# Kernel optimization log

Measured on AMD Instinct MI355X. Metric: run time of the kernel, lower is better.

The kernel has to match this reference:

```python
import jax, jax.numpy as jnp
import numpy as np

B, N0, N1, FD, L, H = 4, 256, 256, 128, 3, 1
NG = N0 + N1            # nodes per graph
N = B * NG              # total nodes
EPS_BN = 1e-5
EPS_SM = 1e-16


def _build_edges():
    def perm_edges(n, off):
        idx = np.arange(n)
        a = np.repeat(idx, n); b = np.tile(idx, n)
        m = a != b
        return np.stack([a[m], b[m]]) + off
    e_intra = np.concatenate([perm_edges(N0, 0), perm_edges(N1, N0)], axis=1)
    a = np.arange(N0); b = np.arange(N0, N0 + N1)
    cross1 = np.stack([np.repeat(a, N1), np.tile(b, N0)])
    cross2 = np.stack([np.repeat(b, N0), np.tile(a, N1)])
    eg = np.concatenate([e_intra, cross1, cross2], axis=1)
    tg = np.concatenate([np.zeros(e_intra.shape[1], np.int32),
                         np.ones(cross1.shape[1] + cross2.shape[1], np.int32)])
    ei = np.concatenate([eg + g * NG for g in range(B)], axis=1).astype(np.int32)
    et = np.tile(tg, B).astype(np.int32)
    return jnp.asarray(ei), jnp.asarray(et)


def setup_inputs() -> dict:
    key = jax.random.key(0)
    ks = jax.random.split(key, 8)
    edge_index, edge_type = _build_edges()
    return {
        'desc0': jax.random.normal(ks[0], (B, FD, N0), jnp.float32),
        'desc1': jax.random.normal(ks[1], (B, FD, N1), jnp.float32),
        'W': jax.random.normal(ks[2], (L, 2, FD, H * FD), jnp.float32) * (1.0 / np.sqrt(FD)),
        'q': jax.random.normal(ks[3], (L, H * FD, H), jnp.float32) * 0.1,
        'k': jax.random.normal(ks[4], (L, H * FD, H), jnp.float32) * 0.1,
        'conv_b': jnp.zeros((L, FD), jnp.float32),
        'lin_W': jax.random.normal(ks[5], (L, FD, 2 * FD), jnp.float32) * (1.0 / np.sqrt(2 * FD)),
        'lin_b': jnp.zeros((L, FD), jnp.float32),
        'gamma': jnp.ones((L, FD), jnp.float32),
        'beta': jnp.zeros((L, FD), jnp.float32),
        'edge_index': edge_index,
        'edge_type': edge_type,
    }


def _forward(desc0, desc1, W, q, k, conv_b, lin_W, lin_b, gamma, beta, edge_index, edge_type):
    # x: [B, NG, FD] -> flattened batch graph [N, FD]
    x = jnp.concatenate([desc0, desc1], axis=2)        # [B, FD, NG]
    x = jnp.transpose(x, (0, 2, 1)).reshape(N, FD)
    src, dst = edge_index[0], edge_index[1]
    nlayers = W.shape[0]
    heads = q.shape[2]
    for l in range(nlayers):
        # relation-specific node projections (equiv to per-edge bmm with weight[edge_type])
        proj = jnp.einsum('nf,rfo->nro', x, W[l])       # [N, 2, H*FD]
        out_i = proj[dst, edge_type]                    # [E, H*FD]
        out_j = proj[src, edge_type]                    # [E, H*FD]
        alpha = jax.nn.leaky_relu(out_i @ q[l] + out_j @ k[l], 0.2)  # [E, H]
        # softmax over incoming edges of each destination node (across-relation)
        amax = jax.ops.segment_max(alpha, dst, num_segments=N)
        ex = jnp.exp(alpha - amax[dst])
        denom = jax.ops.segment_sum(ex, dst, num_segments=N)
        att = ex / (denom[dst] + EPS_SM)                # [E, H]
        msg = (att[:, :, None] * out_j.reshape(-1, heads, FD)).reshape(-1, heads * FD)
        agg = jax.ops.segment_sum(msg, dst, num_segments=N).reshape(N, heads, FD)
        m1 = jax.nn.relu(agg.mean(axis=1) + conv_b[l])  # concat=False -> mean over heads
        m2 = jnp.concatenate([x, m1], axis=1) @ lin_W[l].T + lin_b[l]
        mu = m2.mean(axis=0)
        var = ((m2 - mu) ** 2).mean(axis=0)             # biased var (BatchNorm training)
        m3 = (m2 - mu) / jnp.sqrt(var + EPS_BN) * gamma[l] + beta[l]
        x = x + m3
    x = x.reshape(B, NG, FD).transpose(0, 2, 1)         # [B, FD, NG]
    return x


def reference(desc0, desc1, W, q, k, conv_b, lin_W, lin_b, gamma, beta, edge_index, edge_type):
    x = _forward(desc0, desc1, W, q, k, conv_b, lin_W, lin_b, gamma, beta, edge_index, edge_type)
    return x[:, :, :N0], x[:, :, N0:]
```

## Files before the change

kernel.cpp:

```cpp
#include <hip/hip_runtime.h>

#define FD  128
#define NN  2048

#define OFF_X     0
#define OFF_PROJ  262144
#define OFF_QS    786432
#define OFF_KS    790528
#define OFF_M2    794624
#define OFF_SUMS  1056768
#define OFF_LWT   1057536

__device__ __forceinline__ void proj_qsks(
    const float* __restrict__ W, const float* __restrict__ qv,
    const float* __restrict__ kv, float* __restrict__ ws,
    int l, int n0, int t, const float (*xs)[FD],
    float (*redp)[256], float* red)
{
    int kh = t >> 8, tp = t & 255;
    int rsel = tp >> 7, o = tp & 127;
    const float* Wl = W + ((size_t)(l*2 + rsel)*FD)*FD + o;
    float acc[4] = {0.f, 0.f, 0.f, 0.f};
    int kbase = kh * 64;
    for (int k4 = kbase; k4 < kbase + 64; k4 += 4) {
        float w0 = Wl[(k4+0)*FD], w1 = Wl[(k4+1)*FD];
        float w2 = Wl[(k4+2)*FD], w3 = Wl[(k4+3)*FD];
#pragma unroll
        for (int r = 0; r < 4; r++) {
            float4 xq = *(const float4*)&xs[r][k4];
            acc[r] += xq.x*w0 + xq.y*w1 + xq.z*w2 + xq.w*w3;
        }
    }
    if (kh == 1) {
#pragma unroll
        for (int r = 0; r < 4; r++) redp[r][tp] = acc[r];
    }
    __syncthreads();
    if (t < 256) {
#pragma unroll
        for (int r = 0; r < 4; r++) acc[r] += redp[r][tp];
#pragma unroll
        for (int r = 0; r < 4; r++)
            ws[OFF_PROJ + (size_t)(n0 + r)*256 + tp] = acc[r];

        float qq = qv[l*FD + o], kq = kv[l*FD + o];
        int lane = t & 63, w = t >> 6;
#pragma unroll
        for (int r = 0; r < 4; r++) {
            float vq = acc[r]*qq, vk = acc[r]*kq;
            for (int off = 32; off; off >>= 1) {
                vq += __shfl_xor(vq, off, 64);
                vk += __shfl_xor(vk, off, 64);
            }
            if (lane == 0) { red[w*8 + r*2] = vq; red[w*8 + r*2 + 1] = vk; }
        }
    }
    __syncthreads();
    if (t < 16) {
        int r = t & 3, rs = (t >> 2) & 1, wh = t >> 3;
        float v = red[(rs*2)*8 + r*2 + wh] + red[(rs*2 + 1)*8 + r*2 + wh];
        if (wh == 0) ws[OFF_QS + rs*NN + n0 + r] = v;
        else         ws[OFF_KS + rs*NN + n0 + r] = v;
    }
}

__global__ __launch_bounds__(512, 4) void k_pre(
    const float* __restrict__ d0, const float* __restrict__ d1,
    const float* __restrict__ W,  const float* __restrict__ qv,
    const float* __restrict__ kv, const float* __restrict__ linW,
    float* __restrict__ ws)
{
    int bid = blockIdx.x, t = threadIdx.x;
    if (bid >= 512) {
        if (bid < 536) {
            int vb = bid - 512;
#pragma unroll
            for (int i = 0; i < 8; i++) {
                int e = vb*4096 + i*512 + t;
                int l = e >> 15, rem = e & 32767;
                int o = rem >> 8, c = rem & 255;
                ws[OFF_LWT + l*32768 + c*FD + o] = linW[e];
            }
        } else {
            for (int i = t; i < 768; i += 512) ws[OFF_SUMS + i] = 0.f;
        }
        return;
    }
    __shared__ __attribute__((aligned(16))) float xs[4][FD];
    __shared__ float redp[4][256];
    __shared__ float red[32];
    int n0 = bid * 4;
    {
        int row = t >> 7, f = t & 127;
        int n = n0 + row, gg = n >> 9, ii = n & 511;
        float v = (ii < 256) ? d0[gg*32768 + f*256 + ii]
                             : d1[gg*32768 + f*256 + (ii - 256)];
        xs[row][f] = v;
        ws[OFF_X + (size_t)n*FD + f] = v;
    }
    __syncthreads();
    proj_qsks(W, qv, kv, ws, 0, n0, t, xs, redp, red);
}

__global__ __launch_bounds__(512, 4) void k_bp(
    const float* __restrict__ W,     const float* __restrict__ qv,
    const float* __restrict__ kv,    const float* __restrict__ gamma,
    const float* __restrict__ beta,  float* __restrict__ ws, int l)
{
    __shared__ float scale[FD], shift[FD];
    __shared__ __attribute__((aligned(16))) float xs[4][FD];
    __shared__ float redp[4][256];
    __shared__ float red[32];
    int bid = blockIdx.x, t = threadIdx.x;
    int lp = l - 1;
    if (t < FD) {
        float mu  = ws[OFF_SUMS + lp*256 + t] * (1.f/2048.f);
        float var = ws[OFF_SUMS + lp*256 + 128 + t] * (1.f/2048.f) - mu*mu;
        float rs  = rsqrtf(var + 1e-5f);
        float gm  = gamma[lp*FD + t], bt = beta[lp*FD + t];
        scale[t] = gm * rs;
        shift[t] = bt - mu * gm * rs;
    }
    __syncthreads();
    int n0 = bid * 4;
    {
        int row = t >> 7, f = t & 127;
        size_t e = (size_t)(n0 + row)*FD + f;
        float xv = ws[OFF_X + e] + ws[OFF_M2 + e]*scale[f] + shift[f];
        xs[row][f] = xv;
        ws[OFF_X + e] = xv;
    }
    __syncthreads();
    proj_qsks(W, qv, kv, ws, l, n0, t, xs, redp, red);
}

__global__ __launch_bounds__(512, 4) void k_attn(
    const float* __restrict__ convb, const float* __restrict__ linb,
    float* __restrict__ ws, int l)
{
    __shared__ __attribute__((aligned(16))) float att[4*512];
    __shared__ __attribute__((aligned(16))) float redB[16*4*128];
    __shared__ __attribute__((aligned(16))) float cat[4*256];
    __shared__ float r1[FD], r2[FD];

    int bid = blockIdx.x, t = threadIdx.x;
    int dstbase = bid * 4;
    int g = dstbase >> 9, dloc0 = dstbase & 511;
    int Gd = (dloc0 >= 256) ? 1 : 0;

    if (t < 256) {
        int d = t >> 6, p = t & 63;
        int dloc = dloc0 + d;
        float q0 = ws[OFF_QS + dstbase + d];
        float q1 = ws[OFF_QS + NN + dstbase + d];
        float sc[8];
#pragma unroll
        for (int j = 0; j < 8; j++) {
            int s = p + j*64;
            int ts = (s < 256) ? Gd : 1 - Gd;
            float a = (ts ? q1 : q0) + ws[OFF_KS + ts*NN + g*512 + s];
            a = a > 0.f ? a : 0.2f*a;
            sc[j] = (s == dloc) ? -1e30f : a;
        }
        float lm = sc[0];
#pragma unroll
        for (int j = 1; j < 8; j++) lm = fmaxf(lm, sc[j]);
        for (int off = 32; off; off >>= 1) lm = fmaxf(lm, __shfl_xor(lm, off, 64));
        float ex[8], lsum = 0.f;
#pragma unroll
        for (int j = 0; j < 8; j++) { ex[j] = __expf(sc[j] - lm); lsum += ex[j]; }
        for (int off = 32; off; off >>= 1) lsum += __shfl_xor(lsum, off, 64);
        float inv = 1.f / (lsum + 1e-16f);
#pragma unroll
        for (int j = 0; j < 8; j++) att[d*512 + p + j*64] = ex[j]*inv;
    } else if (t < 384) {
        r1[t - 256] = 0.f;
    } else {
        r2[t - 384] = 0.f;
    }
    __syncthreads();

    int f4 = t & 31, sq = t >> 5;
    {
        int ts = (sq < 8) ? Gd : 1 - Gd;
        const float* P = ws + OFF_PROJ + (size_t)(g*512)*256 + ts*128 + f4*4;
        float acc[4][4];
#pragma unroll
        for (int d2 = 0; d2 < 4; d2++)
#pragma unroll
            for (int j = 0; j < 4; j++) acc[d2][j] = 0.f;
        int s0 = sq * 32;
#pragma unroll 4
        for (int i = 0; i < 32; i++) {
            int s = s0 + i;
            float4 p4 = *(const float4*)&P[(size_t)s*256];
            float b0 = att[0*512 + s], b1 = att[1*512 + s];
            float b2 = att[2*512 + s], b3 = att[3*512 + s];
            acc[0][0] += b0*p4.x; acc[0][1] += b0*p4.y; acc[0][2] += b0*p4.z; acc[0][3] += b0*p4.w;
            acc[1][0] += b1*p4.x; acc[1][1] += b1*p4.y; acc[1][2] += b1*p4.z; acc[1][3] += b1*p4.w;
            acc[2][0] += b2*p4.x; acc[2][1] += b2*p4.y; acc[2][2] += b2*p4.z; acc[2][3] += b2*p4.w;
            acc[3][0] += b3*p4.x; acc[3][1] += b3*p4.y; acc[3][2] += b3*p4.z; acc[3][3] += b3*p4.w;
        }
#pragma unroll
        for (int d2 = 0; d2 < 4; d2++)
            *(float4*)&redB[(sq*4 + d2)*128 + f4*4] =
                make_float4(acc[d2][0], acc[d2][1], acc[d2][2], acc[d2][3]);
    }
    __syncthreads();

    {
        int d2 = t >> 7, f = t & 127;
        float agg = 0.f;
#pragma unroll
        for (int sqi = 0; sqi < 16; sqi++) agg += redB[(sqi*4 + d2)*128 + f];
        float m1v = fmaxf(agg + convb[l*FD + f], 0.f);
        cat[d2*256 + FD + f] = m1v;
        cat[d2*256 + f] = ws[OFF_X + (size_t)(dstbase + d2)*FD + f];
    }
    __syncthreads();

    {
        const float* lwt = ws + OFF_LWT + l*32768 + f4*4;
        float mac[4][4];
#pragma unroll
        for (int d2 = 0; d2 < 4; d2++)
#pragma unroll
            for (int j = 0; j < 4; j++) mac[d2][j] = 0.f;
        int c0 = sq * 16;
#pragma unroll 4
        for (int i = 0; i < 16; i++) {
            int c = c0 + i;
            float4 w4 = *(const float4*)&lwt[c*128];
            float c0v = cat[0*256 + c], c1v = cat[1*256 + c];
            float c2v = cat[2*256 + c], c3v = cat[3*256 + c];
            mac[0][0] += c0v*w4.x; mac[0][1] += c0v*w4.y; mac[0][2] += c0v*w4.z; mac[0][3] += c0v*w4.w;
            mac[1][0] += c1v*w4.x; mac[1][1] += c1v*w4.y; mac[1][2] += c1v*w4.z; mac[1][3] += c1v*w4.w;
            mac[2][0] += c2v*w4.x; mac[2][1] += c2v*w4.y; mac[2][2] += c2v*w4.z; mac[2][3] += c2v*w4.w;
            mac[3][0] += c3v*w4.x; mac[3][1] += c3v*w4.y; mac[3][2] += c3v*w4.z; mac[3][3] += c3v*w4.w;
        }
#pragma unroll
        for (int d2 = 0; d2 < 4; d2++)
            *(float4*)&redB[(sq*4 + d2)*128 + f4*4] =
                make_float4(mac[d2][0], mac[d2][1], mac[d2][2], mac[d2][3]);
    }
    __syncthreads();

    {
        int d2 = t >> 7, o = t & 127;
        float m2v = linb[l*FD + o];
#pragma unroll
        for (int sqi = 0; sqi < 16; sqi++) m2v += redB[(sqi*4 + d2)*128 + o];
        ws[OFF_M2 + (size_t)(dstbase + d2)*FD + o] = m2v;
        atomicAdd(&r1[o], m2v);
        atomicAdd(&r2[o], m2v*m2v);
    }
    __syncthreads();
    if (t < 128) {
        atomicAdd(&ws[OFF_SUMS + l*256 + t],       r1[t]);
        atomicAdd(&ws[OFF_SUMS + l*256 + 128 + t], r2[t]);
    }
}

__global__ __launch_bounds__(256) void k_bnout(
    const float* __restrict__ gamma, const float* __restrict__ beta,
    float* __restrict__ ws, float* __restrict__ out)
{
    __shared__ float scale[FD], shift[FD];
    int bid = blockIdx.x, t = threadIdx.x;
    if (t < FD) {
        float mu  = ws[OFF_SUMS + 2*256 + t] * (1.f/2048.f);
        float var = ws[OFF_SUMS + 2*256 + 128 + t] * (1.f/2048.f) - mu*mu;
        float rs  = rsqrtf(var + 1e-5f);
        float gm  = gamma[2*FD + t], bt = beta[2*FD + t];
        scale[t] = gm * rs;
        shift[t] = bt - mu * gm * rs;
    }
    __syncthreads();
#pragma unroll
    for (int i = 0; i < 2; i++) {
        int idx = bid*512 + i*256 + t;
        int f = idx & 127, n = idx >> 7;
        float v = ws[OFF_X + idx] + ws[OFF_M2 + idx]*scale[f] + shift[f];
        int gg = n >> 9, ii = n & 511;
        int off = (ii < 256) ? (gg*32768 + f*256 + ii)
                             : (131072 + gg*32768 + f*256 + (ii - 256));
        out[off] = v;
    }
}

extern "C" void kernel_launch(void* const* d_in, const int* in_sizes, int n_in,
                              void* d_out, int out_size, void* d_ws, size_t ws_size,
                              hipStream_t stream) {
    (void)in_sizes; (void)n_in; (void)out_size; (void)ws_size;
    const float* desc0 = (const float*)d_in[0];
    const float* desc1 = (const float*)d_in[1];
    const float* W     = (const float*)d_in[2];
    const float* q     = (const float*)d_in[3];
    const float* kk    = (const float*)d_in[4];
    const float* convb = (const float*)d_in[5];
    const float* linW  = (const float*)d_in[6];
    const float* linb  = (const float*)d_in[7];
    const float* gamma = (const float*)d_in[8];
    const float* beta  = (const float*)d_in[9];
    float* ws  = (float*)d_ws;
    float* out = (float*)d_out;

    hipLaunchKernelGGL(k_pre,  dim3(537), dim3(512), 0, stream, desc0, desc1, W, q, kk, linW, ws);
    hipLaunchKernelGGL(k_attn, dim3(512), dim3(512), 0, stream, convb, linb, ws, 0);
    hipLaunchKernelGGL(k_bp,   dim3(512), dim3(512), 0, stream, W, q, kk, gamma, beta, ws, 1);
    hipLaunchKernelGGL(k_attn, dim3(512), dim3(512), 0, stream, convb, linb, ws, 1);
    hipLaunchKernelGGL(k_bp,   dim3(512), dim3(512), 0, stream, W, q, kk, gamma, beta, ws, 2);
    hipLaunchKernelGGL(k_attn, dim3(512), dim3(512), 0, stream, convb, linb, ws, 2);
    hipLaunchKernelGGL(k_bnout, dim3(512), dim3(256), 0, stream, gamma, beta, ws, out);
}
```

Measured before the change: 186.6 us.

## Fuse attention, BatchNorm and next-layer projection via cooperative grid barrier

Merges the per-layer attention kernel with the following BatchNorm-apply and q/k projection into one cooperative kernel. A global atomic counter barrier waits for all blocks' BatchNorm sums, which removes separate launches and the M2 round trip through global memory. It also transposes the attention and concat buffers in shared memory so the inner loops can use float4 reads, and halves the partial-sum buffer with a two-stage reduction. The spin barrier requires all 512 blocks to be co-resident; if the cooperative launch fails, the code falls back to a split path of kernels.

```diff
diff --git a/kernel.cpp b/kernel.cpp
--- a/kernel.cpp
+++ b/kernel.cpp
@@ -7,11 +7,12 @@
 #define OFF_PROJ  262144
 #define OFF_QS    786432
 #define OFF_KS    790528
-#define OFF_M2    794624
-#define OFF_SUMS  1056768
-#define OFF_LWT   1057536
-
-__device__ __forceinline__ void proj_qsks(
+#define OFF_SUMS  794624
+#define OFF_LWT   795392
+#define OFF_M2    893696
+#define OFF_CNT   1155840
+
+__device__ __forceinline__ void proj_qsks512(
     const float* __restrict__ W, const float* __restrict__ qv,
     const float* __restrict__ kv, float* __restrict__ ws,
     int l, int n0, int t, const float (*xs)[FD],
@@ -83,6 +84,7 @@
             }
         } else {
             for (int i = t; i < 768; i += 512) ws[OFF_SUMS + i] = 0.f;
+            if (t < 3) ((unsigned*)(ws + OFF_CNT))[t] = 0u;
         }
         return;
     }
@@ -99,51 +101,14 @@
         ws[OFF_X + (size_t)n*FD + f] = v;
     }
     __syncthreads();
-    proj_qsks(W, qv, kv, ws, 0, n0, t, xs, redp, red);
-}
-
-__global__ __launch_bounds__(512, 4) void k_bp(
-    const float* __restrict__ W,     const float* __restrict__ qv,
-    const float* __restrict__ kv,    const float* __restrict__ gamma,
-    const float* __restrict__ beta,  float* __restrict__ ws, int l)
-{
-    __shared__ float scale[FD], shift[FD];
-    __shared__ __attribute__((aligned(16))) float xs[4][FD];
-    __shared__ float redp[4][256];
-    __shared__ float red[32];
-    int bid = blockIdx.x, t = threadIdx.x;
-    int lp = l - 1;
-    if (t < FD) {
-        float mu  = ws[OFF_SUMS + lp*256 + t] * (1.f/2048.f);
-        float var = ws[OFF_SUMS + lp*256 + 128 + t] * (1.f/2048.f) - mu*mu;
-        float rs  = rsqrtf(var + 1e-5f);
-        float gm  = gamma[lp*FD + t], bt = beta[lp*FD + t];
-        scale[t] = gm * rs;
-        shift[t] = bt - mu * gm * rs;
-    }
-    __syncthreads();
-    int n0 = bid * 4;
-    {
-        int row = t >> 7, f = t & 127;
-        size_t e = (size_t)(n0 + row)*FD + f;
-        float xv = ws[OFF_X + e] + ws[OFF_M2 + e]*scale[f] + shift[f];
-        xs[row][f] = xv;
-        ws[OFF_X + e] = xv;
-    }
-    __syncthreads();
-    proj_qsks(W, qv, kv, ws, l, n0, t, xs, redp, red);
-}
-
-__global__ __launch_bounds__(512, 4) void k_attn(
+    proj_qsks512(W, qv, kv, ws, 0, n0, t, xs, redp, red);
+}
+
+__device__ __forceinline__ float attn_core512(
     const float* __restrict__ convb, const float* __restrict__ linb,
-    float* __restrict__ ws, int l)
-{
-    __shared__ __attribute__((aligned(16))) float att[4*512];
-    __shared__ __attribute__((aligned(16))) float redB[16*4*128];
-    __shared__ __attribute__((aligned(16))) float cat[4*256];
-    __shared__ float r1[FD], r2[FD];
-
-    int bid = blockIdx.x, t = threadIdx.x;
+    float* __restrict__ ws, int l, int bid, int t,
+    float* attT, float* redB, float* catT, float* r1, float* r2)
+{
     int dstbase = bid * 4;
     int g = dstbase >> 9, dloc0 = dstbase & 511;
     int Gd = (dloc0 >= 256) ? 1 : 0;
@@ -172,7 +137,7 @@
         for (int off = 32; off; off >>= 1) lsum += __shfl_xor(lsum, off, 64);
         float inv = 1.f / (lsum + 1e-16f);
 #pragma unroll
-        for (int j = 0; j < 8; j++) att[d*512 + p + j*64] = ex[j]*inv;
+        for (int j = 0; j < 8; j++) attT[(p + j*64)*4 + d] = ex[j]*inv;
     } else if (t < 384) {
         r1[t - 256] = 0.f;
     } else {
@@ -181,30 +146,40 @@
     __syncthreads();
 
     int f4 = t & 31, sq = t >> 5;
+    float acc[4][4];
+#pragma unroll
+    for (int d2 = 0; d2 < 4; d2++)
+#pragma unroll
+        for (int j = 0; j < 4; j++) acc[d2][j] = 0.f;
     {
         int ts = (sq < 8) ? Gd : 1 - Gd;
         const float* P = ws + OFF_PROJ + (size_t)(g*512)*256 + ts*128 + f4*4;
-        float acc[4][4];
-#pragma unroll
-        for (int d2 = 0; d2 < 4; d2++)
-#pragma unroll
-            for (int j = 0; j < 4; j++) acc[d2][j] = 0.f;
         int s0 = sq * 32;
 #pragma unroll 4
         for (int i = 0; i < 32; i++) {
             int s = s0 + i;
             float4 p4 = *(const float4*)&P[(size_t)s*256];
-            float b0 = att[0*512 + s], b1 = att[1*512 + s];
-            float b2 = att[2*512 + s], b3 = att[3*512 + s];
-            acc[0][0] += b0*p4.x; acc[0][1] += b0*p4.y; acc[0][2] += b0*p4.z; acc[0][3] += b0*p4.w;
-            acc[1][0] += b1*p4.x; acc[1][1] += b1*p4.y; acc[1][2] += b1*p4.z; acc[1][3] += b1*p4.w;
-            acc[2][0] += b2*p4.x; acc[2][1] += b2*p4.y; acc[2][2] += b2*p4.z; acc[2][3] += b2*p4.w;
-            acc[3][0] += b3*p4.x; acc[3][1] += b3*p4.y; acc[3][2] += b3*p4.z; acc[3][3] += b3*p4.w;
-        }
+            float4 b4 = *(const float4*)&attT[s*4];
+            acc[0][0] += b4.x*p4.x; acc[0][1] += b4.x*p4.y; acc[0][2] += b4.x*p4.z; acc[0][3] += b4.x*p4.w;
+            acc[1][0] += b4.y*p4.x; acc[1][1] += b4.y*p4.y; acc[1][2] += b4.y*p4.z; acc[1][3] += b4.y*p4.w;
+            acc[2][0] += b4.z*p4.x; acc[2][1] += b4.z*p4.y; acc[2][2] += b4.z*p4.z; acc[2][3] += b4.z*p4.w;
+            acc[3][0] += b4.w*p4.x; acc[3][1] += b4.w*p4.y; acc[3][2] += b4.w*p4.z; acc[3][3] += b4.w*p4.w;
+        }
+    }
+    if (sq >= 8) {
 #pragma unroll
         for (int d2 = 0; d2 < 4; d2++)
+            *(float4*)&redB[((sq - 8)*4 + d2)*128 + f4*4] =
+                make_float4(acc[d2][0], acc[d2][1], acc[d2][2], acc[d2][3]);
+    }
+    __syncthreads();
+    if (sq < 8) {
+#pragma unroll
+        for (int d2 = 0; d2 < 4; d2++) {
+            float4 p4 = *(const float4*)&redB[(sq*4 + d2)*128 + f4*4];
             *(float4*)&redB[(sq*4 + d2)*128 + f4*4] =
-                make_float4(acc[d2][0], acc[d2][1], acc[d2][2], acc[d2][3]);
+                make_float4(acc[d2][0]+p4.x, acc[d2][1]+p4.y, acc[d2][2]+p4.z, acc[d2][3]+p4.w);
+        }
     }
     __syncthreads();
 
@@ -212,79 +187,166 @@
         int d2 = t >> 7, f = t & 127;
         float agg = 0.f;
 #pragma unroll
-        for (int sqi = 0; sqi < 16; sqi++) agg += redB[(sqi*4 + d2)*128 + f];
+        for (int sqi = 0; sqi < 8; sqi++) agg += redB[(sqi*4 + d2)*128 + f];
         float m1v = fmaxf(agg + convb[l*FD + f], 0.f);
-        cat[d2*256 + FD + f] = m1v;
-        cat[d2*256 + f] = ws[OFF_X + (size_t)(dstbase + d2)*FD + f];
-    }
-    __syncthreads();
-
+        catT[(FD + f)*4 + d2] = m1v;
+        catT[f*4 + d2]        = ws[OFF_X + (size_t)(dstbase + d2)*FD + f];
+    }
+    __syncthreads();
+
+#pragma unroll
+    for (int d2 = 0; d2 < 4; d2++)
+#pragma unroll
+        for (int j = 0; j < 4; j++) acc[d2][j] = 0.f;
     {
         const float* lwt = ws + OFF_LWT + l*32768 + f4*4;
-        float mac[4][4];
-#pragma unroll
-        for (int d2 = 0; d2 < 4; d2++)
-#pragma unroll
-            for (int j = 0; j < 4; j++) mac[d2][j] = 0.f;
         int c0 = sq * 16;
 #pragma unroll 4
         for (int i = 0; i < 16; i++) {
             int c = c0 + i;
             float4 w4 = *(const float4*)&lwt[c*128];
-            float c0v = cat[0*256 + c], c1v = cat[1*256 + c];
-            float c2v = cat[2*256 + c], c3v = cat[3*256 + c];
-            mac[0][0] += c0v*w4.x; mac[0][1] += c0v*w4.y; mac[0][2] += c0v*w4.z; mac[0][3] += c0v*w4.w;
-            mac[1][0] += c1v*w4.x; mac[1][1] += c1v*w4.y; mac[1][2] += c1v*w4.z; mac[1][3] += c1v*w4.w;
-            mac[2][0] += c2v*w4.x; mac[2][1] += c2v*w4.y; mac[2][2] += c2v*w4.z; mac[2][3] += c2v*w4.w;
-            mac[3][0] += c3v*w4.x; mac[3][1] += c3v*w4.y; mac[3][2] += c3v*w4.z; mac[3][3] += c3v*w4.w;
-        }
+            float4 c4 = *(const float4*)&catT[c*4];
+            acc[0][0] += c4.x*w4.x; acc[0][1] += c4.x*w4.y; acc[0][2] += c4.x*w4.z; acc[0][3] += c4.x*w4.w;
+            acc[1][0] += c4.y*w4.x; acc[1][1] += c4.y*w4.y; acc[1][2] += c4.y*w4.z; acc[1][3] += c4.y*w4.w;
+            acc[2][0] += c4.z*w4.x; acc[2][1] += c4.z*w4.y; acc[2][2] += c4.z*w4.z; acc[2][3] += c4.z*w4.w;
+            acc[3][0] += c4.w*w4.x; acc[3][1] += c4.w*w4.y; acc[3][2] += c4.w*w4.z; acc[3][3] += c4.w*w4.w;
+        }
+    }
+    if (sq >= 8) {
 #pragma unroll
         for (int d2 = 0; d2 < 4; d2++)
+            *(float4*)&redB[((sq - 8)*4 + d2)*128 + f4*4] =
+                make_float4(acc[d2][0], acc[d2][1], acc[d2][2], acc[d2][3]);
+    }
+    __syncthreads();
+    if (sq < 8) {
+#pragma unroll
+        for (int d2 = 0; d2 < 4; d2++) {
+            float4 p4 = *(const float4*)&redB[(sq*4 + d2)*128 + f4*4];
             *(float4*)&redB[(sq*4 + d2)*128 + f4*4] =
-                make_float4(mac[d2][0], mac[d2][1], mac[d2][2], mac[d2][3]);
-    }
-    __syncthreads();
-
-    {
-        int d2 = t >> 7, o = t & 127;
-        float m2v = linb[l*FD + o];
-#pragma unroll
-        for (int sqi = 0; sqi < 16; sqi++) m2v += redB[(sqi*4 + d2)*128 + o];
-        ws[OFF_M2 + (size_t)(dstbase + d2)*FD + o] = m2v;
-        atomicAdd(&r1[o], m2v);
-        atomicAdd(&r2[o], m2v*m2v);
-    }
+                make_float4(acc[d2][0]+p4.x, acc[d2][1]+p4.y, acc[d2][2]+p4.z, acc[d2][3]+p4.w);
+        }
+    }
+    __syncthreads();
+
+    int d2 = t >> 7, o = t & 127;
+    float m2v = linb[l*FD + o];
+#pragma unroll
+    for (int sqi = 0; sqi < 8; sqi++) m2v += redB[(sqi*4 + d2)*128 + o];
+    atomicAdd(&r1[o], m2v);
+    atomicAdd(&r2[o], m2v*m2v);
     __syncthreads();
     if (t < 128) {
         atomicAdd(&ws[OFF_SUMS + l*256 + t],       r1[t]);
         atomicAdd(&ws[OFF_SUMS + l*256 + 128 + t], r2[t]);
     }
-}
-
-__global__ __launch_bounds__(256) void k_bnout(
-    const float* __restrict__ gamma, const float* __restrict__ beta,
-    float* __restrict__ ws, float* __restrict__ out)
-{
+    return m2v;
+}
+
+__global__ __launch_bounds__(512, 4) void k_layer(
+    const float* __restrict__ W,     const float* __restrict__ qv,
+    const float* __restrict__ kv,    const float* __restrict__ convb,
+    const float* __restrict__ linb,  const float* __restrict__ gamma,
+    const float* __restrict__ beta,  float* __restrict__ ws,
+    float* __restrict__ out,         int l, int last)
+{
+    __shared__ __attribute__((aligned(16))) float attT[512*4];
+    __shared__ __attribute__((aligned(16))) float redB[8*4*128];
+    __shared__ __attribute__((aligned(16))) float catT[256*4];
+    __shared__ float r1[FD], r2[FD];
     __shared__ float scale[FD], shift[FD];
+    __shared__ float red[32];
+
     int bid = blockIdx.x, t = threadIdx.x;
-    if (t < FD) {
-        float mu  = ws[OFF_SUMS + 2*256 + t] * (1.f/2048.f);
-        float var = ws[OFF_SUMS + 2*256 + 128 + t] * (1.f/2048.f) - mu*mu;
+    float m2v = attn_core512(convb, linb, ws, l, bid, t, attT, redB, catT, r1, r2);
+    __syncthreads();
+
+    if (t == 0) {
+        __threadfence();
+        unsigned* cnt = (unsigned*)(ws + OFF_CNT) + l;
+        atomicAdd(cnt, 1u);
+        while (atomicAdd(cnt, 0u) < 512u) __builtin_amdgcn_s_sleep(8);
+    }
+    __syncthreads();
+
+    if (t < 128) {
+        float s1 = atomicAdd(&ws[OFF_SUMS + l*256 + t],       0.f);
+        float s2 = atomicAdd(&ws[OFF_SUMS + l*256 + 128 + t], 0.f);
+        float mu  = s1 * (1.f/2048.f);
+        float var = s2 * (1.f/2048.f) - mu*mu;
         float rs  = rsqrtf(var + 1e-5f);
-        float gm  = gamma[2*FD + t], bt = beta[2*FD + t];
+        float gm  = gamma[l*FD + t], bt = beta[l*FD + t];
         scale[t] = gm * rs;
         shift[t] = bt - mu * gm * rs;
     }
     __syncthreads();
-#pragma unroll
-    for (int i = 0; i < 2; i++) {
-        int idx = bid*512 + i*256 + t;
-        int f = idx & 127, n = idx >> 7;
-        float v = ws[OFF_X + idx] + ws[OFF_M2 + idx]*scale[f] + shift[f];
-        int gg = n >> 9, ii = n & 511;
-        int off = (ii < 256) ? (gg*32768 + f*256 + ii)
-                             : (131072 + gg*32768 + f*256 + (ii - 256));
-        out[off] = v;
+
+    int dstbase = bid * 4;
+    int d2 = t >> 7, o = t & 127;
+    float xnew = catT[o*4 + d2] + m2v*scale[o] + shift[o];
+    if (!last) {
+        ws[OFF_X + (size_t)(dstbase + d2)*FD + o] = xnew;
+        float (*xs)[FD] = (float (*)[FD])attT;
+        xs[d2][o] = xnew;
+        __syncthreads();
+        proj_qsks512(W, qv, kv, ws, l + 1, dstbase, t, xs,
+                     (float (*)[256])redB, red);
+    } else {
+        int n = dstbase + d2, gg = n >> 9, ii = n & 511;
+        int off = (ii < 256) ? (gg*32768 + o*256 + ii)
+                             : (131072 + gg*32768 + o*256 + (ii - 256));
+        out[off] = xnew;
+    }
+}
+
+__global__ __launch_bounds__(512, 4) void k_attn_s(
+    const float* __restrict__ convb, const float* __restrict__ linb,
+    float* __restrict__ ws, int l)
+{
+    __shared__ __attribute__((aligned(16))) float attT[512*4];
+    __shared__ __attribute__((aligned(16))) float redB[8*4*128];
+    __shared__ __attribute__((aligned(16))) float catT[256*4];
+    __shared__ float r1[FD], r2[FD];
+    int bid = blockIdx.x, t = threadIdx.x;
+    float m2v = attn_core512(convb, linb, ws, l, bid, t, attT, redB, catT, r1, r2);
+    int d2 = t >> 7, o = t & 127;
+    ws[OFF_M2 + (size_t)(bid*4 + d2)*FD + o] = m2v;
+}
+
+__global__ __launch_bounds__(512, 4) void k_bnproj(
+    const float* __restrict__ W,     const float* __restrict__ qv,
+    const float* __restrict__ kv,    const float* __restrict__ gamma,
+    const float* __restrict__ beta,  float* __restrict__ ws,
+    float* __restrict__ out,         int l, int last)
+{
+    __shared__ float scale[FD], shift[FD];
+    __shared__ __attribute__((aligned(16))) float xs[4][FD];
+    __shared__ float redp[4][256];
+    __shared__ float red[32];
+    int bid = blockIdx.x, t = threadIdx.x;
+    if (t < 128) {
+        float mu  = ws[OFF_SUMS + l*256 + t] * (1.f/2048.f);
+        float var = ws[OFF_SUMS + l*256 + 128 + t] * (1.f/2048.f) - mu*mu;
+        float rs  = rsqrtf(var + 1e-5f);
+        float gm  = gamma[l*FD + t], bt = beta[l*FD + t];
+        scale[t] = gm * rs;
+        shift[t] = bt - mu * gm * rs;
+    }
+    __syncthreads();
+    int dstbase = bid * 4;
+    int d2 = t >> 7, o = t & 127;
+    size_t e = (size_t)(dstbase + d2)*FD + o;
+    float xnew = ws[OFF_X + e] + ws[OFF_M2 + e]*scale[o] + shift[o];
+    if (!last) {
+        ws[OFF_X + e] = xnew;
+        xs[d2][o] = xnew;
+        __syncthreads();
+        proj_qsks512(W, qv, kv, ws, l + 1, dstbase, t, xs, redp, red);
+    } else {
+        int n = dstbase + d2, gg = n >> 9, ii = n & 511;
+        int off = (ii < 256) ? (gg*32768 + o*256 + ii)
+                             : (131072 + gg*32768 + o*256 + (ii - 256));
+        out[off] = xnew;
     }
 }
 
@@ -305,11 +367,31 @@
     float* ws  = (float*)d_ws;
     float* out = (float*)d_out;
 
-    hipLaunchKernelGGL(k_pre,  dim3(537), dim3(512), 0, stream, desc0, desc1, W, q, kk, linW, ws);
-    hipLaunchKernelGGL(k_attn, dim3(512), dim3(512), 0, stream, convb, linb, ws, 0);
-    hipLaunchKernelGGL(k_bp,   dim3(512), dim3(512), 0, stream, W, q, kk, gamma, beta, ws, 1);
-    hipLaunchKernelGGL(k_attn, dim3(512), dim3(512), 0, stream, convb, linb, ws, 1);
-    hipLaunchKernelGGL(k_bp,   dim3(512), dim3(512), 0, stream, W, q, kk, gamma, beta, ws, 2);
-    hipLaunchKernelGGL(k_attn, dim3(512), dim3(512), 0, stream, convb, linb, ws, 2);
-    hipLaunchKernelGGL(k_bnout, dim3(512), dim3(256), 0, stream, gamma, beta, ws, out);
-}
+    hipLaunchKernelGGL(k_pre, dim3(537), dim3(512), 0, stream,
+                       desc0, desc1, W, q, kk, linW, ws);
+
+    int l0 = 0, last0 = 0;
+    void* args0[] = { (void*)&W, (void*)&q, (void*)&kk, (void*)&convb,
+                      (void*)&linb, (void*)&gamma, (void*)&beta,
+                      (void*)&ws, (void*)&out, (void*)&l0, (void*)&last0 };
+    hipError_t err = hipLaunchCooperativeKernel((const void*)k_layer, dim3(512),
+                                                dim3(512), args0, 0, stream);
+    if (err == hipSuccess) {
+        for (int l = 1; l < 3; l++) {
+            int larg = l, lastarg = (l == 2) ? 1 : 0;
+            void* args[] = { (void*)&W, (void*)&q, (void*)&kk, (void*)&convb,
+                             (void*)&linb, (void*)&gamma, (void*)&beta,
+                             (void*)&ws, (void*)&out, (void*)&larg, (void*)&lastarg };
+            hipLaunchCooperativeKernel((const void*)k_layer, dim3(512), dim3(512),
+                                       args, 0, stream);
+        }
+    } else {
+        for (int l = 0; l < 3; l++) {
+            int lastarg = (l == 2) ? 1 : 0;
+            hipLaunchKernelGGL(k_attn_s, dim3(512), dim3(512), 0, stream,
+                               convb, linb, ws, l);
+            hipLaunchKernelGGL(k_bnproj, dim3(512), dim3(512), 0, stream,
+                               W, q, kk, gamma, beta, ws, out, l, lastarg);
+        }
+    }
+}
```

New measurement: 348.6 us. 1.87x slower.

## Process eight nodes per block with swizzled block-to-node mapping

Applied to the files above, without the earlier changes.

Each block now handles 8 destination nodes instead of 4 in the projection and attention kernels, which halves the grid to 256 blocks and doubles reuse of each loaded W, proj and linW element. The attention kernel's cross-thread reduction becomes a two-stage pairwise add in shared memory so the larger tile still fits. Block indices are swizzled so neighbouring blocks cover different graphs, and the workspace offsets are reordered. In exchange each block uses more registers and shared memory, occupancy is lowered to 2 blocks per unit, and 256 blocks may underfill a 256-CU device.

```diff
diff --git a/kernel.cpp b/kernel.cpp
--- a/kernel.cpp
+++ b/kernel.cpp
@@ -7,11 +7,17 @@
 #define OFF_PROJ  262144
 #define OFF_QS    786432
 #define OFF_KS    790528
-#define OFF_M2    794624
-#define OFF_SUMS  1056768
-#define OFF_LWT   1057536
-
-__device__ __forceinline__ void proj_qsks(
+#define OFF_SUMS  794624
+#define OFF_LWT   795392
+#define OFF_M2    893696
+
+__device__ __forceinline__ int swizzle_n0(int bid) {
+    int g    = (bid & 7) >> 1;
+    int slot = ((bid >> 3) << 1) | (bid & 1);
+    return g*512 + slot*8;
+}
+
+__device__ __forceinline__ void proj_qsks8(
     const float* __restrict__ W, const float* __restrict__ qv,
     const float* __restrict__ kv, float* __restrict__ ws,
     int l, int n0, int t, const float (*xs)[FD],
@@ -20,60 +26,62 @@
     int kh = t >> 8, tp = t & 255;
     int rsel = tp >> 7, o = tp & 127;
     const float* Wl = W + ((size_t)(l*2 + rsel)*FD)*FD + o;
-    float acc[4] = {0.f, 0.f, 0.f, 0.f};
+    float acc[8];
+#pragma unroll
+    for (int r = 0; r < 8; r++) acc[r] = 0.f;
     int kbase = kh * 64;
     for (int k4 = kbase; k4 < kbase + 64; k4 += 4) {
         float w0 = Wl[(k4+0)*FD], w1 = Wl[(k4+1)*FD];
         float w2 = Wl[(k4+2)*FD], w3 = Wl[(k4+3)*FD];
 #pragma unroll
-        for (int r = 0; r < 4; r++) {
+        for (int r = 0; r < 8; r++) {
             float4 xq = *(const float4*)&xs[r][k4];
             acc[r] += xq.x*w0 + xq.y*w1 + xq.z*w2 + xq.w*w3;
         }
     }
     if (kh == 1) {
 #pragma unroll
-        for (int r = 0; r < 4; r++) redp[r][tp] = acc[r];
+        for (int r = 0; r < 8; r++) redp[r][tp] = acc[r];
     }
     __syncthreads();
     if (t < 256) {
 #pragma unroll
-        for (int r = 0; r < 4; r++) acc[r] += redp[r][tp];
-#pragma unroll
-        for (int r = 0; r < 4; r++)
+        for (int r = 0; r < 8; r++) acc[r] += redp[r][tp];
+#pragma unroll
+        for (int r = 0; r < 8; r++)
             ws[OFF_PROJ + (size_t)(n0 + r)*256 + tp] = acc[r];
 
         float qq = qv[l*FD + o], kq = kv[l*FD + o];
         int lane = t & 63, w = t >> 6;
 #pragma unroll
-        for (int r = 0; r < 4; r++) {
+        for (int r = 0; r < 8; r++) {
             float vq = acc[r]*qq, vk = acc[r]*kq;
             for (int off = 32; off; off >>= 1) {
                 vq += __shfl_xor(vq, off, 64);
                 vk += __shfl_xor(vk, off, 64);
             }
-            if (lane == 0) { red[w*8 + r*2] = vq; red[w*8 + r*2 + 1] = vk; }
-        }
-    }
-    __syncthreads();
-    if (t < 16) {
-        int r = t & 3, rs = (t >> 2) & 1, wh = t >> 3;
-        float v = red[(rs*2)*8 + r*2 + wh] + red[(rs*2 + 1)*8 + r*2 + wh];
+            if (lane == 0) { red[w*16 + r*2] = vq; red[w*16 + r*2 + 1] = vk; }
+        }
+    }
+    __syncthreads();
+    if (t < 32) {
+        int r = t & 7, rs = (t >> 3) & 1, wh = t >> 4;
+        float v = red[(rs*2)*16 + r*2 + wh] + red[(rs*2 + 1)*16 + r*2 + wh];
         if (wh == 0) ws[OFF_QS + rs*NN + n0 + r] = v;
         else         ws[OFF_KS + rs*NN + n0 + r] = v;
     }
 }
 
-__global__ __launch_bounds__(512, 4) void k_pre(
+__global__ __launch_bounds__(512, 2) void k_pre(
     const float* __restrict__ d0, const float* __restrict__ d1,
     const float* __restrict__ W,  const float* __restrict__ qv,
     const float* __restrict__ kv, const float* __restrict__ linW,
     float* __restrict__ ws)
 {
     int bid = blockIdx.x, t = threadIdx.x;
-    if (bid >= 512) {
-        if (bid < 536) {
-            int vb = bid - 512;
+    if (bid >= 256) {
+        if (bid < 280) {
+            int vb = bid - 256;
 #pragma unroll
             for (int i = 0; i < 8; i++) {
                 int e = vb*4096 + i*512 + t;
@@ -86,12 +94,14 @@
         }
         return;
     }
-    __shared__ __attribute__((aligned(16))) float xs[4][FD];
-    __shared__ float redp[4][256];
-    __shared__ float red[32];
-    int n0 = bid * 4;
-    {
-        int row = t >> 7, f = t & 127;
+    __shared__ __attribute__((aligned(16))) float xs[8][FD];
+    __shared__ float redp[8][256];
+    __shared__ float red[64];
+    int n0 = swizzle_n0(bid);
+#pragma unroll
+    for (int i = 0; i < 2; i++) {
+        int idx = t + i*512;
+        int row = idx >> 7, f = idx & 127;
         int n = n0 + row, gg = n >> 9, ii = n & 511;
         float v = (ii < 256) ? d0[gg*32768 + f*256 + ii]
                              : d1[gg*32768 + f*256 + (ii - 256)];
@@ -99,21 +109,21 @@
         ws[OFF_X + (size_t)n*FD + f] = v;
     }
     __syncthreads();
-    proj_qsks(W, qv, kv, ws, 0, n0, t, xs, redp, red);
-}
-
-__global__ __launch_bounds__(512, 4) void k_bp(
+    proj_qsks8(W, qv, kv, ws, 0, n0, t, xs, redp, red);
+}
+
+__global__ __launch_bounds__(512, 2) void k_bp(
     const float* __restrict__ W,     const float* __restrict__ qv,
     const float* __restrict__ kv,    const float* __restrict__ gamma,
     const float* __restrict__ beta,  float* __restrict__ ws, int l)
 {
     __shared__ float scale[FD], shift[FD];
-    __shared__ __attribute__((aligned(16))) float xs[4][FD];
-    __shared__ float redp[4][256];
-    __shared__ float red[32];
+    __shared__ __attribute__((aligned(16))) float xs[8][FD];
+    __shared__ float redp[8][256];
+    __shared__ float red[64];
     int bid = blockIdx.x, t = threadIdx.x;
     int lp = l - 1;
-    if (t < FD) {
+    if (t < 128) {
         float mu  = ws[OFF_SUMS + lp*256 + t] * (1.f/2048.f);
         float var = ws[OFF_SUMS + lp*256 + 128 + t] * (1.f/2048.f) - mu*mu;
         float rs  = rsqrtf(var + 1e-5f);
@@ -122,33 +132,35 @@
         shift[t] = bt - mu * gm * rs;
     }
     __syncthreads();
-    int n0 = bid * 4;
-    {
-        int row = t >> 7, f = t & 127;
+    int n0 = swizzle_n0(bid);
+#pragma unroll
+    for (int i = 0; i < 2; i++) {
+        int idx = t + i*512;
+        int row = idx >> 7, f = idx & 127;
         size_t e = (size_t)(n0 + row)*FD + f;
         float xv = ws[OFF_X + e] + ws[OFF_M2 + e]*scale[f] + shift[f];
         xs[row][f] = xv;
         ws[OFF_X + e] = xv;
     }
     __syncthreads();
-    proj_qsks(W, qv, kv, ws, l, n0, t, xs, redp, red);
-}
-
-__global__ __launch_bounds__(512, 4) void k_attn(
+    proj_qsks8(W, qv, kv, ws, l, n0, t, xs, redp, red);
+}
+
+__global__ __launch_bounds__(512, 2) void k_attn(
     const float* __restrict__ convb, const float* __restrict__ linb,
     float* __restrict__ ws, int l)
 {
-    __shared__ __attribute__((aligned(16))) float att[4*512];
-    __shared__ __attribute__((aligned(16))) float redB[16*4*128];
-    __shared__ __attribute__((aligned(16))) float cat[4*256];
+    __shared__ __attribute__((aligned(16))) float att[8*512];
+    __shared__ __attribute__((aligned(16))) float redB[8*8*128];
+    __shared__ __attribute__((aligned(16))) float cat[8*256];
     __shared__ float r1[FD], r2[FD];
 
     int bid = blockIdx.x, t = threadIdx.x;
-    int dstbase = bid * 4;
+    int dstbase = swizzle_n0(bid);
     int g = dstbase >> 9, dloc0 = dstbase & 511;
     int Gd = (dloc0 >= 256) ? 1 : 0;
 
-    if (t < 256) {
+    {
         int d = t >> 6, p = t & 63;
         int dloc = dloc0 + d;
         float q0 = ws[OFF_QS + dstbase + d];
@@ -173,86 +185,114 @@
         float inv = 1.f / (lsum + 1e-16f);
 #pragma unroll
         for (int j = 0; j < 8; j++) att[d*512 + p + j*64] = ex[j]*inv;
-    } else if (t < 384) {
-        r1[t - 256] = 0.f;
-    } else {
-        r2[t - 384] = 0.f;
+        if (t < 128) r1[t] = 0.f;
+        else if (t < 256) r2[t - 128] = 0.f;
     }
     __syncthreads();
 
     int f4 = t & 31, sq = t >> 5;
+    float acc[8][4];
+#pragma unroll
+    for (int d2 = 0; d2 < 8; d2++)
+#pragma unroll
+        for (int j = 0; j < 4; j++) acc[d2][j] = 0.f;
     {
         int ts = (sq < 8) ? Gd : 1 - Gd;
         const float* P = ws + OFF_PROJ + (size_t)(g*512)*256 + ts*128 + f4*4;
-        float acc[4][4];
-#pragma unroll
-        for (int d2 = 0; d2 < 4; d2++)
-#pragma unroll
-            for (int j = 0; j < 4; j++) acc[d2][j] = 0.f;
         int s0 = sq * 32;
 #pragma unroll 4
         for (int i = 0; i < 32; i++) {
             int s = s0 + i;
             float4 p4 = *(const float4*)&P[(size_t)s*256];
-            float b0 = att[0*512 + s], b1 = att[1*512 + s];
-            float b2 = att[2*512 + s], b3 = att[3*512 + s];
-            acc[0][0] += b0*p4.x; acc[0][1] += b0*p4.y; acc[0][2] += b0*p4.z; acc[0][3] += b0*p4.w;
-            acc[1][0] += b1*p4.x; acc[1][1] += b1*p4.y; acc[1][2] += b1*p4.z; acc[1][3] += b1*p4.w;
-            acc[2][0] += b2*p4.x; acc[2][1] += b2*p4.y; acc[2][2] += b2*p4.z; acc[2][3] += b2*p4.w;
-            acc[3][0] += b3*p4.x; acc[3][1] += b3*p4.y; acc[3][2] += b3*p4.z; acc[3][3] += b3*p4.w;
-        }
-#pragma unroll
-        for (int d2 = 0; d2 < 4; d2++)
-            *(float4*)&redB[(sq*4 + d2)*128 + f4*4] =
+#pragma unroll
+            for (int d2 = 0; d2 < 8; d2++) {
+                float b = att[d2*512 + s];
+                acc[d2][0] += b*p4.x; acc[d2][1] += b*p4.y;
+                acc[d2][2] += b*p4.z; acc[d2][3] += b*p4.w;
+            }
+        }
+    }
+    if (sq >= 8) {
+#pragma unroll
+        for (int d2 = 0; d2 < 8; d2++)
+            *(float4*)&redB[((sq - 8)*8 + d2)*128 + f4*4] =
                 make_float4(acc[d2][0], acc[d2][1], acc[d2][2], acc[d2][3]);
     }
     __syncthreads();
-
-    {
-        int d2 = t >> 7, f = t & 127;
-        float agg = 0.f;
-#pragma unroll
-        for (int sqi = 0; sqi < 16; sqi++) agg += redB[(sqi*4 + d2)*128 + f];
-        float m1v = fmaxf(agg + convb[l*FD + f], 0.f);
-        cat[d2*256 + FD + f] = m1v;
-        cat[d2*256 + f] = ws[OFF_X + (size_t)(dstbase + d2)*FD + f];
-    }
-    __syncthreads();
-
+    if (sq < 8) {
+#pragma unroll
+        for (int d2 = 0; d2 < 8; d2++) {
+            float4 p4 = *(const float4*)&redB[(sq*8 + d2)*128 + f4*4];
+            *(float4*)&redB[(sq*8 + d2)*128 + f4*4] =
+                make_float4(acc[d2][0]+p4.x, acc[d2][1]+p4.y, acc[d2][2]+p4.z, acc[d2][3]+p4.w);
+        }
+    }
+    __syncthreads();
+
+    {
+        int dh = t >> 7, f = t & 127;
+#pragma unroll
+        for (int half = 0; half < 2; half++) {
+            int d2 = dh + half*4;
+            float agg = 0.f;
+#pragma unroll
+            for (int cc = 0; cc < 8; cc++) agg += redB[(cc*8 + d2)*128 + f];
+            float m1v = fmaxf(agg + convb[l*FD + f], 0.f);
+            cat[d2*256 + FD + f] = m1v;
+            cat[d2*256 + f] = ws[OFF_X + (size_t)(dstbase + d2)*FD + f];
+        }
+    }
+    __syncthreads();
+
+#pragma unroll
+    for (int d2 = 0; d2 < 8; d2++)
+#pragma unroll
+        for (int j = 0; j < 4; j++) acc[d2][j] = 0.f;
     {
         const float* lwt = ws + OFF_LWT + l*32768 + f4*4;
-        float mac[4][4];
-#pragma unroll
-        for (int d2 = 0; d2 < 4; d2++)
-#pragma unroll
-            for (int j = 0; j < 4; j++) mac[d2][j] = 0.f;
         int c0 = sq * 16;
 #pragma unroll 4
         for (int i = 0; i < 16; i++) {
             int c = c0 + i;
             float4 w4 = *(const float4*)&lwt[c*128];
-            float c0v = cat[0*256 + c], c1v = cat[1*256 + c];
-            float c2v = cat[2*256 + c], c3v = cat[3*256 + c];
-            mac[0][0] += c0v*w4.x; mac[0][1] += c0v*w4.y; mac[0][2] += c0v*w4.z; mac[0][3] += c0v*w4.w;
-            mac[1][0] += c1v*w4.x; mac[1][1] += c1v*w4.y; mac[1][2] += c1v*w4.z; mac[1][3] += c1v*w4.w;
-            mac[2][0] += c2v*w4.x; mac[2][1] += c2v*w4.y; mac[2][2] += c2v*w4.z; mac[2][3] += c2v*w4.w;
-            mac[3][0] += c3v*w4.x; mac[3][1] += c3v*w4.y; mac[3][2] += c3v*w4.z; mac[3][3] += c3v*w4.w;
-        }
-#pragma unroll
-        for (int d2 = 0; d2 < 4; d2++)
-            *(float4*)&redB[(sq*4 + d2)*128 + f4*4] =
-                make_float4(mac[d2][0], mac[d2][1], mac[d2][2], mac[d2][3]);
-    }
-    __syncthreads();
-
-    {
-        int d2 = t >> 7, o = t & 127;
-        float m2v = linb[l*FD + o];
-#pragma unroll
-        for (int sqi = 0; sqi < 16; sqi++) m2v += redB[(sqi*4 + d2)*128 + o];
-        ws[OFF_M2 + (size_t)(dstbase + d2)*FD + o] = m2v;
-        atomicAdd(&r1[o], m2v);
-        atomicAdd(&r2[o], m2v*m2v);
+#pragma unroll
+            for (int d2 = 0; d2 < 8; d2++) {
+                float cv = cat[d2*256 + c];
+                acc[d2][0] += cv*w4.x; acc[d2][1] += cv*w4.y;
+                acc[d2][2] += cv*w4.z; acc[d2][3] += cv*w4.w;
+            }
+        }
+    }
+    if (sq >= 8) {
+#pragma unroll
+        for (int d2 = 0; d2 < 8; d2++)
+            *(float4*)&redB[((sq - 8)*8 + d2)*128 + f4*4] =
+                make_float4(acc[d2][0], acc[d2][1], acc[d2][2], acc[d2][3]);
+    }
+    __syncthreads();
+    if (sq < 8) {
+#pragma unroll
+        for (int d2 = 0; d2 < 8; d2++) {
+            float4 p4 = *(const float4*)&redB[(sq*8 + d2)*128 + f4*4];
+            *(float4*)&redB[(sq*8 + d2)*128 + f4*4] =
+                make_float4(acc[d2][0]+p4.x, acc[d2][1]+p4.y, acc[d2][2]+p4.z, acc[d2][3]+p4.w);
+        }
+    }
+    __syncthreads();
+
+    {
+        int dh = t >> 7, o = t & 127;
+        float lb = linb[l*FD + o];
+#pragma unroll
+        for (int half = 0; half < 2; half++) {
+            int d2 = dh + half*4;
+            float m2v = lb;
+#pragma unroll
+            for (int cc = 0; cc < 8; cc++) m2v += redB[(cc*8 + d2)*128 + o];
+            ws[OFF_M2 + (size_t)(dstbase + d2)*FD + o] = m2v;
+            atomicAdd(&r1[o], m2v);
+            atomicAdd(&r2[o], m2v*m2v);
+        }
     }
     __syncthreads();
     if (t < 128) {
@@ -267,7 +307,7 @@
 {
     __shared__ float scale[FD], shift[FD];
     int bid = blockIdx.x, t = threadIdx.x;
-    if (t < FD) {
+    if (t < 128) {
         float mu  = ws[OFF_SUMS + 2*256 + t] * (1.f/2048.f);
         float var = ws[OFF_SUMS + 2*256 + 128 + t] * (1.f/2048.f) - mu*mu;
         float rs  = rsqrtf(var + 1e-5f);
@@ -305,11 +345,11 @@
     float* ws  = (float*)d_ws;
     float* out = (float*)d_out;
 
-    hipLaunchKernelGGL(k_pre,  dim3(537), dim3(512), 0, stream, desc0, desc1, W, q, kk, linW, ws);
-    hipLaunchKernelGGL(k_attn, dim3(512), dim3(512), 0, stream, convb, linb, ws, 0);
-    hipLaunchKernelGGL(k_bp,   dim3(512), dim3(512), 0, stream, W, q, kk, gamma, beta, ws, 1);
-    hipLaunchKernelGGL(k_attn, dim3(512), dim3(512), 0, stream, convb, linb, ws, 1);
-    hipLaunchKernelGGL(k_bp,   dim3(512), dim3(512), 0, stream, W, q, kk, gamma, beta, ws, 2);
-    hipLaunchKernelGGL(k_attn, dim3(512), dim3(512), 0, stream, convb, linb, ws, 2);
+    hipLaunchKernelGGL(k_pre,  dim3(281), dim3(512), 0, stream, desc0, desc1, W, q, kk, linW, ws);
+    hipLaunchKernelGGL(k_attn, dim3(256), dim3(512), 0, stream, convb, linb, ws, 0);
+    hipLaunchKernelGGL(k_bp,   dim3(256), dim3(512), 0, stream, W, q, kk, gamma, beta, ws, 1);
+    hipLaunchKernelGGL(k_attn, dim3(256), dim3(512), 0, stream, convb, linb, ws, 1);
+    hipLaunchKernelGGL(k_bp,   dim3(256), dim3(512), 0, stream, W, q, kk, gamma, beta, ws, 2);
+    hipLaunchKernelGGL(k_attn, dim3(256), dim3(512), 0, stream, convb, linb, ws, 2);
     hipLaunchKernelGGL(k_bnout, dim3(512), dim3(256), 0, stream, gamma, beta, ws, out);
 }
```

New measurement: 175.7 us. -5.8%, faster.
